# Optimization experiments

Measured on AMD Instinct MI355X. Metric: run time of the kernel, lower is better.

## Reference

```python
import jax, jax.numpy as jnp
import numpy as np
import math

IN_DIM = 256
OUT_DIM = 256
H = 4
DK = OUT_DIM // H  # 64
N = 40000
E = 300000
T = 2  # node types
R = 3  # relations: 0:(A->B), 1:(B->A), 2:(A->B)


def setup_inputs() -> dict:
    key = jax.random.key(0)
    ks = jax.random.split(key, 24)
    def xavier(k, shape):
        fan_in, fan_out = shape[-2], shape[-1]
        lim = math.sqrt(6.0 / (fan_in + fan_out))
        return jax.random.uniform(k, shape, jnp.float32, -lim, lim)
    inp = {
        "hA": jax.random.normal(ks[0], (N, IN_DIM), jnp.float32),
        "hB": jax.random.normal(ks[1], (N, IN_DIM), jnp.float32),
        "src0": jax.random.randint(ks[2], (E,), 0, N, jnp.int32),
        "dst0": jax.random.randint(ks[3], (E,), 0, N, jnp.int32),
        "src1": jax.random.randint(ks[4], (E,), 0, N, jnp.int32),
        "dst1": jax.random.randint(ks[5], (E,), 0, N, jnp.int32),
        "src2": jax.random.randint(ks[6], (E,), 0, N, jnp.int32),
        "dst2": jax.random.randint(ks[7], (E,), 0, N, jnp.int32),
        # per-node-type linear weights, stacked [T, in, out]
        "Wk": xavier(ks[8], (T, IN_DIM, OUT_DIM)),
        "bk": jnp.zeros((T, OUT_DIM), jnp.float32),
        "Wq": xavier(ks[9], (T, IN_DIM, OUT_DIM)),
        "bq": jnp.zeros((T, OUT_DIM), jnp.float32),
        "Wv": xavier(ks[10], (T, IN_DIM, OUT_DIM)),
        "bv": jnp.zeros((T, OUT_DIM), jnp.float32),
        "Wa": xavier(ks[11], (T, OUT_DIM, OUT_DIM)),
        "ba": jnp.zeros((T, OUT_DIM), jnp.float32),
        "rel_att": xavier(ks[12], (R, H, DK, DK)),
        "rel_msg": xavier(ks[13], (R, H, DK, DK)),
        "rel_pri": jnp.ones((R, H), jnp.float32),
        "skip": jnp.ones((T,), jnp.float32),
    }
    return inp


def _hgt_forward(hA, hB, Wk, bk, Wq, bq, Wv, bv, Wa, ba,
                 rel_att, rel_msg, rel_pri, skip, edges):
    h = [hA, hB]
    sqrt_dk = math.sqrt(DK)

    def proj(W, b, x, t):
        return (x @ W[t] + b[t]).reshape(-1, H, DK)

    def rel_agg(r, s, d, src, dst):
        # relation-specific transforms
        k = jnp.einsum('nhi,hij->nhj', proj(Wk, bk, h[s], s), rel_att[r])
        v = jnp.einsum('nhi,hij->nhj', proj(Wv, bv, h[s], s), rel_msg[r])
        q = proj(Wq, bq, h[d], d)
        nd = h[d].shape[0]
        # per-edge dot-product attention score [E, H]
        score = jnp.einsum('ehd,ehd->eh', q[dst], k[src]) * rel_pri[r] / sqrt_dk
        # edge softmax normalized by destination node
        m = jax.ops.segment_max(score, dst, num_segments=nd)
        e = jnp.exp(score - m[dst])
        denom = jax.ops.segment_sum(e, dst, num_segments=nd)
        attn = e / denom[dst]
        # weighted scatter-sum aggregation -> [nd, H, DK]
        return jax.ops.segment_sum(v[src] * attn[:, :, None], dst, num_segments=nd)

    (src0, dst0), (src1, dst1), (src2, dst2) = edges
    agg0 = rel_agg(0, 0, 1, src0, dst0)  # A -> B
    agg1 = rel_agg(1, 1, 0, src1, dst1)  # B -> A
    agg2 = rel_agg(2, 0, 1, src2, dst2)  # A -> B

    # cross_reducer='mean' over etypes per destination type
    t_A = agg1.reshape(-1, OUT_DIM)
    t_B = ((agg0 + agg2) * 0.5).reshape(-1, OUT_DIM)

    def ts_aggr(t, n_id, h_dst):
        alpha = jax.nn.sigmoid(skip[n_id])
        trans = t @ Wa[n_id] + ba[n_id]  # dropout p=0.0 -> identity
        return trans * alpha + h_dst * (1.0 - alpha)

    out_A = ts_aggr(t_A, 0, hA)
    out_B = ts_aggr(t_B, 1, hB)
    return jnp.stack([out_A, out_B])  # [2, N, OUT_DIM]


def reference(hA, hB, src0, dst0, src1, dst1, src2, dst2,
              Wk, bk, Wq, bq, Wv, bv, Wa, ba,
              rel_att, rel_msg, rel_pri, skip):
    edges = ((src0, dst0), (src1, dst1), (src2, dst2))
    return _hgt_forward(hA, hB, Wk, bk, Wq, bq, Wv, bv, Wa, ba,
                        rel_att, rel_msg, rel_pri, skip, edges)
```

## Files before the change

kernel.cpp:

```cpp
#include <hip/hip_runtime.h>

#define NN 40000
#define EE 300000
#define DIM 256
#define NHD 4
#define CAP 64

typedef __attribute__((ext_vector_type(8))) short bfrag;
typedef __attribute__((ext_vector_type(4))) float fx4;

static __device__ __forceinline__ float bf2f(unsigned short u) {
  union { unsigned int i; float f; } v; v.i = ((unsigned int)u) << 16; return v.f;
}
static __device__ __forceinline__ unsigned short f2bf(float f) {
  union { float f; unsigned int i; } v; v.f = f;
  unsigned int x = v.i;
  return (unsigned short)((x + 0x7fffu + ((x >> 16) & 1u)) >> 16);
}
static __device__ __forceinline__ void unpack4(uint2 u, float f[4]) {
  f[0] = bf2f((unsigned short)(u.x & 0xffffu));
  f[1] = bf2f((unsigned short)(u.x >> 16));
  f[2] = bf2f((unsigned short)(u.y & 0xffffu));
  f[3] = bf2f((unsigned short)(u.y >> 16));
}
static __device__ __forceinline__ void unpackKV(uint4 u, float k[4], float v[4]) {
  k[0] = bf2f((unsigned short)(u.x & 0xffffu)); k[1] = bf2f((unsigned short)(u.x >> 16));
  k[2] = bf2f((unsigned short)(u.y & 0xffffu)); k[3] = bf2f((unsigned short)(u.y >> 16));
  v[0] = bf2f((unsigned short)(u.z & 0xffffu)); v[1] = bf2f((unsigned short)(u.z >> 16));
  v[2] = bf2f((unsigned short)(u.w & 0xffffu)); v[3] = bf2f((unsigned short)(u.w >> 16));
}
static __device__ __forceinline__ void gload_lds16(const unsigned short* g, unsigned short* l) {
  __builtin_amdgcn_global_load_lds((const __attribute__((address_space(1))) void*)g,
                                   (__attribute__((address_space(3))) void*)l, 16, 0, 0);
}

#define LDSBUF 16384
static __device__ __forceinline__ void gemm_core(const unsigned short* __restrict__ X,
                                                 const unsigned short* __restrict__ WT,
                                                 int R0, int C0, int rowMax,
                                                 fx4 acc[4][4],
                                                 unsigned short* lds) {
  const int tid = threadIdx.x;
  const int wave = tid >> 6, lane = tid & 63;
  const int li = lane & 15, lk = lane >> 4;
  const int wr = wave >> 1, wc = wave & 1;
  const int lr = lane >> 3;
  const int swz = ((lane & 7) ^ lr) * 8;

#define STAGE(KT, BUF)                                                          \
  {                                                                             \
    unsigned short* lA = lds + (BUF) * LDSBUF;                                  \
    unsigned short* lB = lA + 8192;                                             \
    const int k0 = (KT) * 64;                                                   \
    _Pragma("unroll")                                                           \
    for (int i = 0; i < 4; ++i) {                                               \
      int g = wave * 4 + i;                                                     \
      int ra = min(R0 + g * 8 + lr, rowMax);                                    \
      gload_lds16(X + (size_t)ra * DIM + k0 + swz, lA + g * 512);               \
      int cb = C0 + g * 8 + lr;                                                 \
      gload_lds16(WT + (size_t)cb * DIM + k0 + swz, lB + g * 512);              \
    }                                                                           \
  }

  STAGE(0, 0);
#pragma unroll
  for (int kt = 0; kt < 4; ++kt) {
    __syncthreads();
    if (kt < 3) STAGE(kt + 1, (kt + 1) & 1);
    unsigned short* lA = lds + (kt & 1) * LDSBUF;
    unsigned short* lB = lA + 8192;
#pragma unroll
    for (int ks = 0; ks < 2; ++ks) {
      bfrag a[4], b[4];
      const int chb = (lk + ks * 4) ^ (li & 7);
#pragma unroll
      for (int mt = 0; mt < 4; ++mt)
        a[mt] = *(const bfrag*)(lA + (wr * 64 + mt * 16 + li) * 64 + chb * 8);
#pragma unroll
      for (int nt = 0; nt < 4; ++nt)
        b[nt] = *(const bfrag*)(lB + (wc * 64 + nt * 16 + li) * 64 + chb * 8);
#pragma unroll
      for (int mt = 0; mt < 4; ++mt)
#pragma unroll
        for (int nt = 0; nt < 4; ++nt)
          acc[mt][nt] = __builtin_amdgcn_mfma_f32_16x16x32_bf16(a[mt], b[nt], acc[mt][nt], 0, 0, 0);
    }
  }
#undef STAGE
}

__global__ __launch_bounds__(256) void cvt_kernel(const float* __restrict__ hA,
                                                  const float* __restrict__ hB,
                                                  unsigned short* __restrict__ XA,
                                                  unsigned short* __restrict__ XB) {
  long id = (long)blockIdx.x * 256 + threadIdx.x;
  const long half = (long)NN * DIM / 8;
  const float4* src; unsigned short* dst; long o;
  if (id < half) { src = (const float4*)hA; dst = XA; o = id; }
  else           { src = (const float4*)hB; dst = XB; o = id - half; }
  float4 a = src[o * 2], b = src[o * 2 + 1];
  uint4 pk;
  pk.x = (unsigned)f2bf(a.x) | ((unsigned)f2bf(a.y) << 16);
  pk.y = (unsigned)f2bf(a.z) | ((unsigned)f2bf(a.w) << 16);
  pk.z = (unsigned)f2bf(b.x) | ((unsigned)f2bf(b.y) << 16);
  pk.w = (unsigned)f2bf(b.z) | ((unsigned)f2bf(b.w) << 16);
  ((uint4*)dst)[o] = pk;
}

__global__ __launch_bounds__(256) void prep_weights(
    const float* __restrict__ Wk, const float* __restrict__ bk,
    const float* __restrict__ Wq, const float* __restrict__ bq,
    const float* __restrict__ Wv, const float* __restrict__ bv,
    const float* __restrict__ Wa,
    const float* __restrict__ rel_att, const float* __restrict__ rel_msg,
    const float* __restrict__ rel_pri,
    unsigned short* __restrict__ WT_A, unsigned short* __restrict__ WT_B,
    unsigned short* __restrict__ WaT, float* __restrict__ biasA, float* __restrict__ biasB) {
  int id = blockIdx.x * 256 + threadIdx.x;
  if (id < 262144) {
    int c = id >> 8, i = id & 255;
    int br = c >> 9, w = c & 511, h = w >> 7, ww = w & 127;
    int iskv = (ww >> 2) & 1;
    int j = (ww >> 3) * 4 + (ww & 3);
    int r = br ? 2 : 0;
    const float* W  = iskv ? Wv : Wk;
    const float* RM = iskv ? rel_msg : rel_att;
    const float* wrow = W + i * 256 + h * 64;
    const float* rm = RM + (size_t)((r * NHD + h) * 64) * 64 + j;
    float s = 0.f;
#pragma unroll 8
    for (int l = 0; l < 64; l++) s += wrow[l] * rm[l * 64];
    if (!iskv) s *= rel_pri[r * NHD + h] * 0.125f;
    WT_A[c * 256 + i] = f2bf(s);
    return;
  }
  id -= 262144;
  if (id < 65536) {
    int c = id >> 8, i = id & 255;
    WT_A[(1024 + c) * 256 + i] = f2bf(Wq[i * 256 + c]);
    return;
  }
  id -= 65536;
  if (id < 131072) {
    int c = id >> 8, i = id & 255;
    int h = c >> 7, ww = c & 127;
    int iskv = (ww >> 2) & 1;
    int j = (ww >> 3) * 4 + (ww & 3);
    const float* W  = iskv ? Wv : Wk;
    const float* RM = iskv ? rel_msg : rel_att;
    const float* wrow = W + 65536 + i * 256 + h * 64;
    const float* rm = RM + (size_t)((1 * NHD + h) * 64) * 64 + j;
    float s = 0.f;
#pragma unroll 8
    for (int l = 0; l < 64; l++) s += wrow[l] * rm[l * 64];
    if (!iskv) s *= rel_pri[1 * NHD + h] * 0.125f;
    WT_B[c * 256 + i] = f2bf(s);
    return;
  }
  id -= 131072;
  if (id < 65536) {
    int c = id >> 8, i = id & 255;
    WT_B[(512 + c) * 256 + i] = f2bf(Wq[65536 + i * 256 + c]);
    return;
  }
  id -= 65536;
  if (id < 131072) {
    int t = id >> 16, rem = id & 65535, c = rem >> 8, i = rem & 255;
    WaT[t * 65536 + c * 256 + i] = f2bf(Wa[t * 65536 + i * 256 + c]);
    return;
  }
  id -= 131072;
  if (id < 2048) {
    if (id < 1280) {
      int c = id; float s;
      if (c < 1024) {
        int br = c >> 9, w = c & 511, h = w >> 7, ww = w & 127;
        int iskv = (ww >> 2) & 1;
        int j = (ww >> 3) * 4 + (ww & 3);
        int r = br ? 2 : 0;
        const float* B  = iskv ? bv : bk;
        const float* RM = iskv ? rel_msg : rel_att;
        s = 0.f;
        for (int l = 0; l < 64; l++)
          s += B[h * 64 + l] * RM[(size_t)((r * NHD + h) * 64 + l) * 64 + j];
        if (!iskv) s *= rel_pri[r * NHD + h] * 0.125f;
      } else s = bq[c - 1024];
      biasA[c] = s;
    } else {
      int c = id - 1280; float s;
      if (c < 512) {
        int h = c >> 7, ww = c & 127;
        int iskv = (ww >> 2) & 1;
        int j = (ww >> 3) * 4 + (ww & 3);
        const float* B  = iskv ? bv : bk;
        const float* RM = iskv ? rel_msg : rel_att;
        s = 0.f;
        for (int l = 0; l < 64; l++)
          s += B[256 + h * 64 + l] * RM[(size_t)((1 * NHD + h) * 64 + l) * 64 + j];
        if (!iskv) s *= rel_pri[1 * NHD + h] * 0.125f;
      } else s = bq[256 + (c - 512)];
      biasB[c] = s;
    }
  }
}

__global__ __launch_bounds__(256) void bucket_build(const int* __restrict__ src0, const int* __restrict__ dst0,
                                                    const int* __restrict__ src1, const int* __restrict__ dst1,
                                                    const int* __restrict__ src2, const int* __restrict__ dst2,
                                                    int* __restrict__ cnt, int* __restrict__ bkt) {
  int e = blockIdx.x * 256 + threadIdx.x;
  if (e >= EE) return;
  int r = blockIdx.y;
  const int* src = r == 0 ? src0 : (r == 1 ? src1 : src2);
  const int* dst = r == 0 ? dst0 : (r == 1 ? dst1 : dst2);
  int d = dst[e];
  int pos = atomicAdd(&cnt[r * NN + d], 1);
  if (pos < CAP) bkt[(size_t)r * NN * CAP + d * CAP + pos] = src[e];
}

__global__ __launch_bounds__(256) void gemm_kvq(const unsigned short* __restrict__ X,
                                                const unsigned short* __restrict__ WT,
                                                const float* __restrict__ bias,
                                                unsigned short* __restrict__ Out, int ldOut) {
  __shared__ unsigned short lds[2 * LDSBUF];
  fx4 acc[4][4] = {};
  const int R0 = blockIdx.x * 128, C0 = blockIdx.y * 128;
  gemm_core(X, WT, R0, C0, NN - 1, acc, lds);
  const int wave = threadIdx.x >> 6, lane = threadIdx.x & 63;
  const int li = lane & 15, lk = lane >> 4;
  const int wr = wave >> 1, wc = wave & 1;
#pragma unroll
  for (int mt = 0; mt < 4; mt++)
#pragma unroll
    for (int nt = 0; nt < 4; nt++) {
      int col = C0 + wc * 64 + nt * 16 + li;
      float bcol = bias[col];
      int rbase = R0 + wr * 64 + mt * 16 + lk * 4;
#pragma unroll
      for (int i = 0; i < 4; i++) {
        int row = rbase + i;
        if (row < NN) Out[(long)row * ldOut + col] = f2bf(acc[mt][nt][i] + bcol);
      }
    }
}

__global__ __launch_bounds__(256) void agg_all(const unsigned short* __restrict__ OutA,
                                               const unsigned short* __restrict__ OutB,
                                               const int* __restrict__ cnt,
                                               const int* __restrict__ bkt,
                                               unsigned short* __restrict__ tA,
                                               unsigned short* __restrict__ tB) {
  int wid = (blockIdx.x * 256 + threadIdx.x) >> 6;
  int lane = threadIdx.x & 63;
  int h = lane >> 4, li = lane & 15;
  int qoff = h * 64 + li * 4;
  int kvoff = h * 128 + li * 8;
  if (wid < NN) {
    int n = wid;
    float q[4]; unpack4(*(const uint2*)(OutB + (size_t)n * 768 + 512 + qoff), q);
    int c0 = min(cnt[n], CAP);
    int c2 = min(cnt[2 * NN + n], CAP);
    int s0 = (lane < c0) ? bkt[(size_t)0 * NN * CAP + n * CAP + lane] : 0;
    int s2 = (lane < c2) ? bkt[(size_t)2 * NN * CAP + n * CAP + lane] : 0;
    float l0 = 0.f, l2 = 0.f;
    float b00 = 0.f, b01 = 0.f, b02 = 0.f, b03 = 0.f;
    float b20 = 0.f, b21 = 0.f, b22 = 0.f, b23 = 0.f;
    int cm = max(c0, c2);
    for (int e = 0; e < cm; ++e) {
      if (e < c0) {
        int src = __builtin_amdgcn_readlane(s0, e);
        uint4 u = *(const uint4*)(OutA + (size_t)src * 1280 + kvoff);
        float kk[4], vv[4]; unpackKV(u, kk, vv);
        float pp = q[0] * kk[0] + q[1] * kk[1] + q[2] * kk[2] + q[3] * kk[3];
        pp += __shfl_xor(pp, 1); pp += __shfl_xor(pp, 2);
        pp += __shfl_xor(pp, 4); pp += __shfl_xor(pp, 8);
        float p = __expf(pp);
        l0 += p; b00 += p * vv[0]; b01 += p * vv[1]; b02 += p * vv[2]; b03 += p * vv[3];
      }
      if (e < c2) {
        int src = __builtin_amdgcn_readlane(s2, e);
        uint4 u = *(const uint4*)(OutA + (size_t)src * 1280 + 512 + kvoff);
        float kk[4], vv[4]; unpackKV(u, kk, vv);
        float pp = q[0] * kk[0] + q[1] * kk[1] + q[2] * kk[2] + q[3] * kk[3];
        pp += __shfl_xor(pp, 1); pp += __shfl_xor(pp, 2);
        pp += __shfl_xor(pp, 4); pp += __shfl_xor(pp, 8);
        float p = __expf(pp);
        l2 += p; b20 += p * vv[0]; b21 += p * vv[1]; b22 += p * vv[2]; b23 += p * vv[3];
      }
    }
    float i0 = (l0 > 0.f) ? 0.5f / l0 : 0.f;
    float i2 = (l2 > 0.f) ? 0.5f / l2 : 0.f;
    float r0 = b00 * i0 + b20 * i2, r1 = b01 * i0 + b21 * i2;
    float r2 = b02 * i0 + b22 * i2, r3 = b03 * i0 + b23 * i2;
    uint2 pk;
    pk.x = (unsigned)f2bf(r0) | ((unsigned)f2bf(r1) << 16);
    pk.y = (unsigned)f2bf(r2) | ((unsigned)f2bf(r3) << 16);
    *(uint2*)(tB + (size_t)n * DIM + qoff) = pk;
  } else if (wid < 2 * NN) {
    int n = wid - NN;
    float q[4]; unpack4(*(const uint2*)(OutA + (size_t)n * 1280 + 1024 + qoff), q);
    int c = min(cnt[NN + n], CAP);
    int s1 = (lane < c) ? bkt[(size_t)1 * NN * CAP + n * CAP + lane] : 0;
    float l = 0.f, a0 = 0.f, a1 = 0.f, a2 = 0.f, a3 = 0.f;
    int e = 0;
    for (; e + 1 < c; e += 2) {
      int sa = __builtin_amdgcn_readlane(s1, e);
      int sb = __builtin_amdgcn_readlane(s1, e + 1);
      uint4 ua = *(const uint4*)(OutB + (size_t)sa * 768 + kvoff);
      uint4 ub = *(const uint4*)(OutB + (size_t)sb * 768 + kvoff);
      float ka[4], va[4], kb[4], vb[4];
      unpackKV(ua, ka, va); unpackKV(ub, kb, vb);
      float pa = q[0] * ka[0] + q[1] * ka[1] + q[2] * ka[2] + q[3] * ka[3];
      float pb = q[0] * kb[0] + q[1] * kb[1] + q[2] * kb[2] + q[3] * kb[3];
      pa += __shfl_xor(pa, 1); pa += __shfl_xor(pa, 2);
      pa += __shfl_xor(pa, 4); pa += __shfl_xor(pa, 8);
      pb += __shfl_xor(pb, 1); pb += __shfl_xor(pb, 2);
      pb += __shfl_xor(pb, 4); pb += __shfl_xor(pb, 8);
      pa = __expf(pa); pb = __expf(pb);
      l += pa; l += pb;
      a0 += pa * va[0]; a1 += pa * va[1]; a2 += pa * va[2]; a3 += pa * va[3];
      a0 += pb * vb[0]; a1 += pb * vb[1]; a2 += pb * vb[2]; a3 += pb * vb[3];
    }
    if (e < c) {
      int sa = __builtin_amdgcn_readlane(s1, e);
      uint4 ua = *(const uint4*)(OutB + (size_t)sa * 768 + kvoff);
      float ka[4], va[4]; unpackKV(ua, ka, va);
      float pa = q[0] * ka[0] + q[1] * ka[1] + q[2] * ka[2] + q[3] * ka[3];
      pa += __shfl_xor(pa, 1); pa += __shfl_xor(pa, 2);
      pa += __shfl_xor(pa, 4); pa += __shfl_xor(pa, 8);
      pa = __expf(pa);
      l += pa;
      a0 += pa * va[0]; a1 += pa * va[1]; a2 += pa * va[2]; a3 += pa * va[3];
    }
    float inv = (l > 0.f) ? 1.f / l : 0.f;
    uint2 pk;
    pk.x = (unsigned)f2bf(a0 * inv) | ((unsigned)f2bf(a1 * inv) << 16);
    pk.y = (unsigned)f2bf(a2 * inv) | ((unsigned)f2bf(a3 * inv) << 16);
    *(uint2*)(tA + (size_t)n * DIM + qoff) = pk;
  }
}

__global__ __launch_bounds__(256) void gemm_final2(const unsigned short* __restrict__ tA,
                                                   const unsigned short* __restrict__ tB,
                                                   const unsigned short* __restrict__ XA,
                                                   const unsigned short* __restrict__ XB,
                                                   const unsigned short* __restrict__ WaT,
                                                   const float* __restrict__ ba,
                                                   const float* __restrict__ skip,
                                                   float* __restrict__ outp) {
  __shared__ unsigned short lds[2 * LDSBUF];
  const int t = blockIdx.z;
  const unsigned short* Tt = t ? tB : tA;
  const unsigned short* hin = t ? XB : XA;
  float* op = outp + (size_t)t * NN * DIM;
  fx4 acc[4][4] = {};
  const int R0 = blockIdx.x * 128, C0 = blockIdx.y * 128;
  gemm_core(Tt, WaT + t * 65536, R0, C0, NN - 1, acc, lds);
  const int wave = threadIdx.x >> 6, lane = threadIdx.x & 63;
  const int li = lane & 15, lk = lane >> 4;
  const int wr = wave >> 1, wc = wave & 1;
  float alpha = 1.f / (1.f + __expf(-skip[t]));
  float beta = 1.f - alpha;
#pragma unroll
  for (int mt = 0; mt < 4; mt++)
#pragma unroll
    for (int nt = 0; nt < 4; nt++) {
      int col = C0 + wc * 64 + nt * 16 + li;
      float bcol = ba[t * 256 + col];
      int rbase = R0 + wr * 64 + mt * 16 + lk * 4;
#pragma unroll
      for (int i = 0; i < 4; i++) {
        int row = rbase + i;
        if (row < NN) {
          float hv = bf2f(hin[(size_t)row * DIM + col]);
          op[(long)row * DIM + col] = (acc[mt][nt][i] + bcol) * alpha + hv * beta;
        }
      }
    }
}

extern "C" void kernel_launch(void* const* d_in, const int* in_sizes, int n_in,
                              void* d_out, int out_size, void* d_ws, size_t ws_size,
                              hipStream_t stream) {
  const float* hA = (const float*)d_in[0];
  const float* hB = (const float*)d_in[1];
  const int* src0 = (const int*)d_in[2];
  const int* dst0 = (const int*)d_in[3];
  const int* src1 = (const int*)d_in[4];
  const int* dst1 = (const int*)d_in[5];
  const int* src2 = (const int*)d_in[6];
  const int* dst2 = (const int*)d_in[7];
  const float* Wk = (const float*)d_in[8];
  const float* bk = (const float*)d_in[9];
  const float* Wq = (const float*)d_in[10];
  const float* bq = (const float*)d_in[11];
  const float* Wv = (const float*)d_in[12];
  const float* bv = (const float*)d_in[13];
  const float* Wa = (const float*)d_in[14];
  const float* ba = (const float*)d_in[15];
  const float* rel_att = (const float*)d_in[16];
  const float* rel_msg = (const float*)d_in[17];
  const float* rel_pri = (const float*)d_in[18];
  const float* skip = (const float*)d_in[19];

  char* w = (char*)d_ws;
  unsigned short* XA   = (unsigned short*)(w);
  unsigned short* XB   = (unsigned short*)(w + 20480000);
  unsigned short* OutA = (unsigned short*)(w + 40960000);
  unsigned short* OutB = (unsigned short*)(w + 143360000);
  unsigned short* WT_A = (unsigned short*)(w + 204800000);
  unsigned short* WT_B = (unsigned short*)(w + 205455360);
  unsigned short* WaT  = (unsigned short*)(w + 205848576);
  float* biasA = (float*)(w + 206110720);
  float* biasB = (float*)(w + 206115840);
  int* cnt  = (int*)(w + 206118912);
  int* bkt  = (int*)(w + 206598912);
  unsigned short* tA = (unsigned short*)(w + 237318912);
  unsigned short* tB = (unsigned short*)(w + 257798912);

  hipMemsetAsync(cnt, 0, 3 * NN * sizeof(int), stream);
  cvt_kernel<<<10000, 256, 0, stream>>>(hA, hB, XA, XB);
  prep_weights<<<2568, 256, 0, stream>>>(Wk, bk, Wq, bq, Wv, bv, Wa,
                                         rel_att, rel_msg, rel_pri,
                                         WT_A, WT_B, WaT, biasA, biasB);
  bucket_build<<<dim3((EE + 255) / 256, 3), 256, 0, stream>>>(src0, dst0, src1, dst1, src2, dst2, cnt, bkt);
  gemm_kvq<<<dim3(313, 10), 256, 0, stream>>>(XA, WT_A, biasA, OutA, 1280);
  gemm_kvq<<<dim3(313, 6), 256, 0, stream>>>(XB, WT_B, biasB, OutB, 768);
  agg_all<<<20000, 256, 0, stream>>>(OutA, OutB, cnt, bkt, tA, tB);
  gemm_final2<<<dim3(313, 2, 2), 256, 0, stream>>>(tA, tB, XA, XB, WaT, ba, skip, (float*)d_out);
}
```

Measured before the change: 441.2 us.

## Restructure GEMMs as full-K panels with XCD swizzle and pipeline aggregation loads

```diff
diff --git a/kernel.cpp b/kernel.cpp
--- a/kernel.cpp
+++ b/kernel.cpp
@@ -5,88 +5,78 @@
 #define DIM 256
 #define NHD 4
 #define CAP 64
+#define LOG2E 1.4426950408889634f
 
 typedef __attribute__((ext_vector_type(8))) short bfrag;
 typedef __attribute__((ext_vector_type(4))) float fx4;
 
-static __device__ __forceinline__ float bf2f(unsigned short u) {
-  union { unsigned int i; float f; } v; v.i = ((unsigned int)u) << 16; return v.f;
+static __device__ __forceinline__ float bflo(unsigned u) {
+  union { unsigned i; float f; } v; v.i = u << 16; return v.f;
+}
+static __device__ __forceinline__ float bfhi(unsigned u) {
+  union { unsigned i; float f; } v; v.i = u & 0xffff0000u; return v.f;
 }
 static __device__ __forceinline__ unsigned short f2bf(float f) {
-  union { float f; unsigned int i; } v; v.f = f;
-  unsigned int x = v.i;
+  union { float f; unsigned i; } v; v.f = f;
+  unsigned x = v.i;
   return (unsigned short)((x + 0x7fffu + ((x >> 16) & 1u)) >> 16);
-}
-static __device__ __forceinline__ void unpack4(uint2 u, float f[4]) {
-  f[0] = bf2f((unsigned short)(u.x & 0xffffu));
-  f[1] = bf2f((unsigned short)(u.x >> 16));
-  f[2] = bf2f((unsigned short)(u.y & 0xffffu));
-  f[3] = bf2f((unsigned short)(u.y >> 16));
-}
-static __device__ __forceinline__ void unpackKV(uint4 u, float k[4], float v[4]) {
-  k[0] = bf2f((unsigned short)(u.x & 0xffffu)); k[1] = bf2f((unsigned short)(u.x >> 16));
-  k[2] = bf2f((unsigned short)(u.y & 0xffffu)); k[3] = bf2f((unsigned short)(u.y >> 16));
-  v[0] = bf2f((unsigned short)(u.z & 0xffffu)); v[1] = bf2f((unsigned short)(u.z >> 16));
-  v[2] = bf2f((unsigned short)(u.w & 0xffffu)); v[3] = bf2f((unsigned short)(u.w >> 16));
 }
 static __device__ __forceinline__ void gload_lds16(const unsigned short* g, unsigned short* l) {
   __builtin_amdgcn_global_load_lds((const __attribute__((address_space(1))) void*)g,
                                    (__attribute__((address_space(3))) void*)l, 16, 0, 0);
 }
 
-#define LDSBUF 16384
-static __device__ __forceinline__ void gemm_core(const unsigned short* __restrict__ X,
-                                                 const unsigned short* __restrict__ WT,
-                                                 int R0, int C0, int rowMax,
-                                                 fx4 acc[4][4],
-                                                 unsigned short* lds) {
-  const int tid = threadIdx.x;
-  const int wave = tid >> 6, lane = tid & 63;
+static __device__ __forceinline__ void panel_core(const unsigned short* __restrict__ X,
+                                                  const unsigned short* __restrict__ WT,
+                                                  int R0, int C0,
+                                                  fx4 acc[4][2], unsigned short* ldsB) {
+  const int tid = threadIdx.x, wave = tid >> 6, lane = tid & 63;
   const int li = lane & 15, lk = lane >> 4;
-  const int wr = wave >> 1, wc = wave & 1;
-  const int lr = lane >> 3;
-  const int swz = ((lane & 7) ^ lr) * 8;
-
-#define STAGE(KT, BUF)                                                          \
-  {                                                                             \
-    unsigned short* lA = lds + (BUF) * LDSBUF;                                  \
-    unsigned short* lB = lA + 8192;                                             \
-    const int k0 = (KT) * 64;                                                   \
-    _Pragma("unroll")                                                           \
-    for (int i = 0; i < 4; ++i) {                                               \
-      int g = wave * 4 + i;                                                     \
-      int ra = min(R0 + g * 8 + lr, rowMax);                                    \
-      gload_lds16(X + (size_t)ra * DIM + k0 + swz, lA + g * 512);               \
-      int cb = C0 + g * 8 + lr;                                                 \
-      gload_lds16(WT + (size_t)cb * DIM + k0 + swz, lB + g * 512);              \
-    }                                                                           \
-  }
-
-  STAGE(0, 0);
-#pragma unroll
-  for (int kt = 0; kt < 4; ++kt) {
-    __syncthreads();
-    if (kt < 3) STAGE(kt + 1, (kt + 1) & 1);
-    unsigned short* lA = lds + (kt & 1) * LDSBUF;
-    unsigned short* lB = lA + 8192;
-#pragma unroll
-    for (int ks = 0; ks < 2; ++ks) {
-      bfrag a[4], b[4];
-      const int chb = (lk + ks * 4) ^ (li & 7);
-#pragma unroll
-      for (int mt = 0; mt < 4; ++mt)
-        a[mt] = *(const bfrag*)(lA + (wr * 64 + mt * 16 + li) * 64 + chb * 8);
-#pragma unroll
-      for (int nt = 0; nt < 4; ++nt)
-        b[nt] = *(const bfrag*)(lB + (wc * 64 + nt * 16 + li) * 64 + chb * 8);
-#pragma unroll
-      for (int mt = 0; mt < 4; ++mt)
-#pragma unroll
-        for (int nt = 0; nt < 4; ++nt)
-          acc[mt][nt] = __builtin_amdgcn_mfma_f32_16x16x32_bf16(a[mt], b[nt], acc[mt][nt], 0, 0, 0);
+  const int wc = wave & 1, wr = wave >> 1;
+  {
+    const int lr = lane >> 5, ch = lane & 31;
+#pragma unroll
+    for (int i = 0; i < 8; ++i) {
+      int g = wave * 8 + i;
+      int col = g * 2 + lr;
+      int sch = ch ^ (col & 7);
+      gload_lds16(WT + (size_t)(C0 + col) * DIM + sch * 8, ldsB + g * 512);
     }
   }
-#undef STAGE
+  bfrag a[4][8];
+#pragma unroll
+  for (int mt = 0; mt < 4; ++mt) {
+    int ra = min(R0 + wr * 64 + mt * 16 + li, NN - 1);
+    const unsigned short* xr = X + (size_t)ra * DIM + lk * 8;
+#pragma unroll
+    for (int ks = 0; ks < 8; ++ks)
+      a[mt][ks] = *(const bfrag*)(xr + ks * 32);
+  }
+  __syncthreads();
+#pragma unroll
+  for (int ks = 0; ks < 8; ++ks) {
+    bfrag b[2];
+#pragma unroll
+    for (int nt = 0; nt < 2; ++nt) {
+      int col = wc * 32 + nt * 16 + li;
+      int chb = (ks * 4 + lk) ^ (col & 7);
+      b[nt] = *(const bfrag*)(ldsB + col * 256 + chb * 8);
+    }
+#pragma unroll
+    for (int mt = 0; mt < 4; ++mt)
+#pragma unroll
+      for (int nt = 0; nt < 2; ++nt)
+        acc[mt][nt] = __builtin_amdgcn_mfma_f32_16x16x32_bf16(a[mt][ks], b[nt], acc[mt][nt], 0, 0, 0);
+  }
+}
+
+static __device__ __forceinline__ void swz_block(int& bx, int& by) {
+  int gx = gridDim.x, nwg = gx * gridDim.y;
+  int lin = blockIdx.y * gx + blockIdx.x;
+  int qq = nwg >> 3, rr = nwg & 7;
+  int xcd = lin & 7, off = lin >> 3;
+  int work = (xcd < rr ? xcd * (qq + 1) : rr * (qq + 1) + (xcd - rr) * qq) + off;
+  bx = work % gx; by = work / gx;
 }
 
 __global__ __launch_bounds__(256) void cvt_kernel(const float* __restrict__ hA,
@@ -130,7 +120,7 @@
     float s = 0.f;
 #pragma unroll 8
     for (int l = 0; l < 64; l++) s += wrow[l] * rm[l * 64];
-    if (!iskv) s *= rel_pri[r * NHD + h] * 0.125f;
+    if (!iskv) s *= rel_pri[r * NHD + h] * 0.125f * LOG2E;
     WT_A[c * 256 + i] = f2bf(s);
     return;
   }
@@ -153,7 +143,7 @@
     float s = 0.f;
 #pragma unroll 8
     for (int l = 0; l < 64; l++) s += wrow[l] * rm[l * 64];
-    if (!iskv) s *= rel_pri[1 * NHD + h] * 0.125f;
+    if (!iskv) s *= rel_pri[1 * NHD + h] * 0.125f * LOG2E;
     WT_B[c * 256 + i] = f2bf(s);
     return;
   }
@@ -183,7 +173,7 @@
         s = 0.f;
         for (int l = 0; l < 64; l++)
           s += B[h * 64 + l] * RM[(size_t)((r * NHD + h) * 64 + l) * 64 + j];
-        if (!iskv) s *= rel_pri[r * NHD + h] * 0.125f;
+        if (!iskv) s *= rel_pri[r * NHD + h] * 0.125f * LOG2E;
       } else s = bq[c - 1024];
       biasA[c] = s;
     } else {
@@ -197,7 +187,7 @@
         s = 0.f;
         for (int l = 0; l < 64; l++)
           s += B[256 + h * 64 + l] * RM[(size_t)((1 * NHD + h) * 64 + l) * 64 + j];
-        if (!iskv) s *= rel_pri[1 * NHD + h] * 0.125f;
+        if (!iskv) s *= rel_pri[1 * NHD + h] * 0.125f * LOG2E;
       } else s = bq[256 + (c - 512)];
       biasB[c] = s;
     }
@@ -218,22 +208,23 @@
   if (pos < CAP) bkt[(size_t)r * NN * CAP + d * CAP + pos] = src[e];
 }
 
-__global__ __launch_bounds__(256) void gemm_kvq(const unsigned short* __restrict__ X,
-                                                const unsigned short* __restrict__ WT,
-                                                const float* __restrict__ bias,
-                                                unsigned short* __restrict__ Out, int ldOut) {
-  __shared__ unsigned short lds[2 * LDSBUF];
-  fx4 acc[4][4] = {};
-  const int R0 = blockIdx.x * 128, C0 = blockIdx.y * 128;
-  gemm_core(X, WT, R0, C0, NN - 1, acc, lds);
+__global__ __launch_bounds__(256, 2) void gemm_kvq(const unsigned short* __restrict__ X,
+                                                   const unsigned short* __restrict__ WT,
+                                                   const float* __restrict__ bias,
+                                                   unsigned short* __restrict__ Out, int ldOut) {
+  __shared__ unsigned short ldsB[16384];
+  int bx, by; swz_block(bx, by);
+  const int R0 = by * 128, C0 = bx * 64;
+  fx4 acc[4][2] = {};
+  panel_core(X, WT, R0, C0, acc, ldsB);
   const int wave = threadIdx.x >> 6, lane = threadIdx.x & 63;
   const int li = lane & 15, lk = lane >> 4;
-  const int wr = wave >> 1, wc = wave & 1;
+  const int wc = wave & 1, wr = wave >> 1;
 #pragma unroll
   for (int mt = 0; mt < 4; mt++)
 #pragma unroll
-    for (int nt = 0; nt < 4; nt++) {
-      int col = C0 + wc * 64 + nt * 16 + li;
+    for (int nt = 0; nt < 2; nt++) {
+      int col = C0 + wc * 32 + nt * 16 + li;
       float bcol = bias[col];
       int rbase = R0 + wr * 64 + mt * 16 + lk * 4;
 #pragma unroll
@@ -242,6 +233,44 @@
         if (row < NN) Out[(long)row * ldOut + col] = f2bf(acc[mt][nt][i] + bcol);
       }
     }
+}
+
+template<int LD>
+static __device__ __forceinline__ void proc_bucket(const unsigned short* __restrict__ Out,
+                                                   int c, int srcs, int kvoff,
+                                                   float q0, float q1, float q2, float q3,
+                                                   float& L, float& A0, float& A1, float& A2, float& A3) {
+  const uint4 Z = {0u, 0u, 0u, 0u};
+  auto ldx = [&](int E) -> uint4 {
+    int s = __builtin_amdgcn_readlane(srcs, E & 63);
+    return *(const uint4*)(Out + (size_t)s * LD + kvoff);
+  };
+  auto proc = [&](uint4 u) {
+    float pp = q0 * bflo(u.x) + q1 * bfhi(u.x) + q2 * bflo(u.y) + q3 * bfhi(u.y);
+    pp += __shfl_xor(pp, 1); pp += __shfl_xor(pp, 2);
+    pp += __shfl_xor(pp, 4); pp += __shfl_xor(pp, 8);
+    float p = exp2f(pp);
+    L += p;
+    A0 += p * bflo(u.z); A1 += p * bfhi(u.z);
+    A2 += p * bflo(u.w); A3 += p * bfhi(u.w);
+  };
+  uint4 e0 = Z, e1 = Z, e2 = Z, e3 = Z;
+  if (0 < c) e0 = ldx(0);
+  if (1 < c) e1 = ldx(1);
+  if (2 < c) e2 = ldx(2);
+  if (3 < c) e3 = ldx(3);
+  for (int e = 0; e < c; e += 4) {
+    uint4 f0 = Z, f1 = Z, f2 = Z, f3 = Z;
+    if (e + 4 < c) f0 = ldx(e + 4);
+    if (e + 5 < c) f1 = ldx(e + 5);
+    if (e + 6 < c) f2 = ldx(e + 6);
+    if (e + 7 < c) f3 = ldx(e + 7);
+    proc(e0);
+    if (e + 1 < c) proc(e1);
+    if (e + 2 < c) proc(e2);
+    if (e + 3 < c) proc(e3);
+    e0 = f0; e1 = f1; e2 = f2; e3 = f3;
+  }
 }
 
 __global__ __launch_bounds__(256) void agg_all(const unsigned short* __restrict__ OutA,
@@ -257,37 +286,16 @@
   int kvoff = h * 128 + li * 8;
   if (wid < NN) {
     int n = wid;
-    float q[4]; unpack4(*(const uint2*)(OutB + (size_t)n * 768 + 512 + qoff), q);
+    uint2 qr = *(const uint2*)(OutB + (size_t)n * 768 + 512 + qoff);
+    float q0 = bflo(qr.x), q1 = bfhi(qr.x), q2 = bflo(qr.y), q3 = bfhi(qr.y);
     int c0 = min(cnt[n], CAP);
     int c2 = min(cnt[2 * NN + n], CAP);
-    int s0 = (lane < c0) ? bkt[(size_t)0 * NN * CAP + n * CAP + lane] : 0;
+    int s0 = (lane < c0) ? bkt[(size_t)n * CAP + lane] : 0;
     int s2 = (lane < c2) ? bkt[(size_t)2 * NN * CAP + n * CAP + lane] : 0;
-    float l0 = 0.f, l2 = 0.f;
-    float b00 = 0.f, b01 = 0.f, b02 = 0.f, b03 = 0.f;
-    float b20 = 0.f, b21 = 0.f, b22 = 0.f, b23 = 0.f;
-    int cm = max(c0, c2);
-    for (int e = 0; e < cm; ++e) {
-      if (e < c0) {
-        int src = __builtin_amdgcn_readlane(s0, e);
-        uint4 u = *(const uint4*)(OutA + (size_t)src * 1280 + kvoff);
-        float kk[4], vv[4]; unpackKV(u, kk, vv);
-        float pp = q[0] * kk[0] + q[1] * kk[1] + q[2] * kk[2] + q[3] * kk[3];
-        pp += __shfl_xor(pp, 1); pp += __shfl_xor(pp, 2);
-        pp += __shfl_xor(pp, 4); pp += __shfl_xor(pp, 8);
-        float p = __expf(pp);
-        l0 += p; b00 += p * vv[0]; b01 += p * vv[1]; b02 += p * vv[2]; b03 += p * vv[3];
-      }
-      if (e < c2) {
-        int src = __builtin_amdgcn_readlane(s2, e);
-        uint4 u = *(const uint4*)(OutA + (size_t)src * 1280 + 512 + kvoff);
-        float kk[4], vv[4]; unpackKV(u, kk, vv);
-        float pp = q[0] * kk[0] + q[1] * kk[1] + q[2] * kk[2] + q[3] * kk[3];
-        pp += __shfl_xor(pp, 1); pp += __shfl_xor(pp, 2);
-        pp += __shfl_xor(pp, 4); pp += __shfl_xor(pp, 8);
-        float p = __expf(pp);
-        l2 += p; b20 += p * vv[0]; b21 += p * vv[1]; b22 += p * vv[2]; b23 += p * vv[3];
-      }
-    }
+    float l0 = 0.f, b00 = 0.f, b01 = 0.f, b02 = 0.f, b03 = 0.f;
+    float l2 = 0.f, b20 = 0.f, b21 = 0.f, b22 = 0.f, b23 = 0.f;
+    proc_bucket<1280>(OutA,       c0, s0, kvoff, q0, q1, q2, q3, l0, b00, b01, b02, b03);
+    proc_bucket<1280>(OutA + 512, c2, s2, kvoff, q0, q1, q2, q3, l2, b20, b21, b22, b23);
     float i0 = (l0 > 0.f) ? 0.5f / l0 : 0.f;
     float i2 = (l2 > 0.f) ? 0.5f / l2 : 0.f;
     float r0 = b00 * i0 + b20 * i2, r1 = b01 * i0 + b21 * i2;
@@ -298,40 +306,12 @@
     *(uint2*)(tB + (size_t)n * DIM + qoff) = pk;
   } else if (wid < 2 * NN) {
     int n = wid - NN;
-    float q[4]; unpack4(*(const uint2*)(OutA + (size_t)n * 1280 + 1024 + qoff), q);
+    uint2 qr = *(const uint2*)(OutA + (size_t)n * 1280 + 1024 + qoff);
+    float q0 = bflo(qr.x), q1 = bfhi(qr.x), q2 = bflo(qr.y), q3 = bfhi(qr.y);
     int c = min(cnt[NN + n], CAP);
-    int s1 = (lane < c) ? bkt[(size_t)1 * NN * CAP + n * CAP + lane] : 0;
+    int s1 = (lane < c) ? bkt[(size_t)NN * CAP + n * CAP + lane] : 0;
     float l = 0.f, a0 = 0.f, a1 = 0.f, a2 = 0.f, a3 = 0.f;
-    int e = 0;
-    for (; e + 1 < c; e += 2) {
-      int sa = __builtin_amdgcn_readlane(s1, e);
-      int sb = __builtin_amdgcn_readlane(s1, e + 1);
-      uint4 ua = *(const uint4*)(OutB + (size_t)sa * 768 + kvoff);
-      uint4 ub = *(const uint4*)(OutB + (size_t)sb * 768 + kvoff);
-      float ka[4], va[4], kb[4], vb[4];
-      unpackKV(ua, ka, va); unpackKV(ub, kb, vb);
-      float pa = q[0] * ka[0] + q[1] * ka[1] + q[2] * ka[2] + q[3] * ka[3];
-      float pb = q[0] * kb[0] + q[1] * kb[1] + q[2] * kb[2] + q[3] * kb[3];
-      pa += __shfl_xor(pa, 1); pa += __shfl_xor(pa, 2);
-      pa += __shfl_xor(pa, 4); pa += __shfl_xor(pa, 8);
-      pb += __shfl_xor(pb, 1); pb += __shfl_xor(pb, 2);
-      pb += __shfl_xor(pb, 4); pb += __shfl_xor(pb, 8);
-      pa = __expf(pa); pb = __expf(pb);
-      l += pa; l += pb;
-      a0 += pa * va[0]; a1 += pa * va[1]; a2 += pa * va[2]; a3 += pa * va[3];
-      a0 += pb * vb[0]; a1 += pb * vb[1]; a2 += pb * vb[2]; a3 += pb * vb[3];
-    }
-    if (e < c) {
-      int sa = __builtin_amdgcn_readlane(s1, e);
-      uint4 ua = *(const uint4*)(OutB + (size_t)sa * 768 + kvoff);
-      float ka[4], va[4]; unpackKV(ua, ka, va);
-      float pa = q[0] * ka[0] + q[1] * ka[1] + q[2] * ka[2] + q[3] * ka[3];
-      pa += __shfl_xor(pa, 1); pa += __shfl_xor(pa, 2);
-      pa += __shfl_xor(pa, 4); pa += __shfl_xor(pa, 8);
-      pa = __expf(pa);
-      l += pa;
-      a0 += pa * va[0]; a1 += pa * va[1]; a2 += pa * va[2]; a3 += pa * va[3];
-    }
+    proc_bucket<768>(OutB, c, s1, kvoff, q0, q1, q2, q3, l, a0, a1, a2, a3);
     float inv = (l > 0.f) ? 1.f / l : 0.f;
     uint2 pk;
     pk.x = (unsigned)f2bf(a0 * inv) | ((unsigned)f2bf(a1 * inv) << 16);
@@ -340,39 +320,41 @@
   }
 }
 
-__global__ __launch_bounds__(256) void gemm_final2(const unsigned short* __restrict__ tA,
-                                                   const unsigned short* __restrict__ tB,
-                                                   const unsigned short* __restrict__ XA,
-                                                   const unsigned short* __restrict__ XB,
-                                                   const unsigned short* __restrict__ WaT,
-                                                   const float* __restrict__ ba,
-                                                   const float* __restrict__ skip,
-                                                   float* __restrict__ outp) {
-  __shared__ unsigned short lds[2 * LDSBUF];
+__global__ __launch_bounds__(256, 2) void gemm_final2(const unsigned short* __restrict__ tA,
+                                                      const unsigned short* __restrict__ tB,
+                                                      const unsigned short* __restrict__ XA,
+                                                      const unsigned short* __restrict__ XB,
+                                                      const unsigned short* __restrict__ WaT,
+                                                      const float* __restrict__ ba,
+                                                      const float* __restrict__ skip,
+                                                      float* __restrict__ outp) {
+  __shared__ unsigned short ldsB[16384];
   const int t = blockIdx.z;
   const unsigned short* Tt = t ? tB : tA;
   const unsigned short* hin = t ? XB : XA;
   float* op = outp + (size_t)t * NN * DIM;
-  fx4 acc[4][4] = {};
-  const int R0 = blockIdx.x * 128, C0 = blockIdx.y * 128;
-  gemm_core(Tt, WaT + t * 65536, R0, C0, NN - 1, acc, lds);
+  int bx, by; swz_block(bx, by);
+  const int R0 = by * 128, C0 = bx * 64;
+  fx4 acc[4][2] = {};
+  panel_core(Tt, WaT + t * 65536, R0, C0, acc, ldsB);
   const int wave = threadIdx.x >> 6, lane = threadIdx.x & 63;
   const int li = lane & 15, lk = lane >> 4;
-  const int wr = wave >> 1, wc = wave & 1;
+  const int wc = wave & 1, wr = wave >> 1;
   float alpha = 1.f / (1.f + __expf(-skip[t]));
   float beta = 1.f - alpha;
 #pragma unroll
   for (int mt = 0; mt < 4; mt++)
 #pragma unroll
-    for (int nt = 0; nt < 4; nt++) {
-      int col = C0 + wc * 64 + nt * 16 + li;
+    for (int nt = 0; nt < 2; nt++) {
+      int col = C0 + wc * 32 + nt * 16 + li;
       float bcol = ba[t * 256 + col];
       int rbase = R0 + wr * 64 + mt * 16 + lk * 4;
 #pragma unroll
       for (int i = 0; i < 4; i++) {
         int row = rbase + i;
         if (row < NN) {
-          float hv = bf2f(hin[(size_t)row * DIM + col]);
+          float hv = bflo((unsigned)hin[(size_t)row * DIM + col] << 0) ;
+          hv = bflo((unsigned)hin[(size_t)row * DIM + col]);
           op[(long)row * DIM + col] = (acc[mt][nt][i] + bcol) * alpha + hv * beta;
         }
       }
@@ -424,8 +406,8 @@
                                          rel_att, rel_msg, rel_pri,
                                          WT_A, WT_B, WaT, biasA, biasB);
   bucket_build<<<dim3((EE + 255) / 256, 3), 256, 0, stream>>>(src0, dst0, src1, dst1, src2, dst2, cnt, bkt);
-  gemm_kvq<<<dim3(313, 10), 256, 0, stream>>>(XA, WT_A, biasA, OutA, 1280);
-  gemm_kvq<<<dim3(313, 6), 256, 0, stream>>>(XB, WT_B, biasB, OutB, 768);
+  gemm_kvq<<<dim3(20, 313), 256, 0, stream>>>(XA, WT_A, biasA, OutA, 1280);
+  gemm_kvq<<<dim3(12, 313), 256, 0, stream>>>(XB, WT_B, biasB, OutB, 768);
   agg_all<<<20000, 256, 0, stream>>>(OutA, OutB, cnt, bkt, tA, tB);
-  gemm_final2<<<dim3(313, 2, 2), 256, 0, stream>>>(tA, tB, XA, XB, WaT, ba, skip, (float*)d_out);
-}
+  gemm_final2<<<dim3(4, 313, 2), 256, 0, stream>>>(tA, tB, XA, XB, WaT, ba, skip, (float*)d_out);
+}
```

Result: slower. 540.5 us (+22.5%).
